# Performance work log

Measured on AMD Instinct MI355X. Metric: run time of the kernel, lower is better.

The kernel has to match this reference:

```python
import jax, jax.numpy as jnp
import numpy as np

B, L_SRC, L_TGT, H = 8, 256, 256, 768
N_SRC_WORDS, N_TGT_WORDS = 128, 128


def setup_inputs() -> dict:
    key = jax.random.key(0)
    k1, k2 = jax.random.split(key, 2)
    L = L_SRC + L_TGT
    tok_h = jax.random.normal(k1, (B, L, H), dtype=jnp.float32)
    attention_mask = jnp.ones((B, L), dtype=jnp.int32)
    # monotone word ids covering exactly N words (ragged spans of ~2 tokens/word)
    src_ids = (jnp.arange(L_SRC) * N_SRC_WORDS // L_SRC).astype(jnp.int64)
    tgt_ids = (jnp.arange(L_TGT) * N_TGT_WORDS // L_TGT).astype(jnp.int64)
    source_word_ids = jnp.broadcast_to(src_ids, (B, L_SRC))
    target_word_ids = jnp.broadcast_to(tgt_ids, (B, L_TGT))
    W = jax.random.normal(k2, (2 * H, 1), dtype=jnp.float32) * 0.02
    b = jnp.zeros((1,), dtype=jnp.float32)
    return dict(tok_h=tok_h, attention_mask=attention_mask,
                source_word_ids=source_word_ids, target_word_ids=target_word_ids,
                W=W, b=b, S=N_SRC_WORDS, T=N_TGT_WORDS)


def _pool_words(tok_h, combined_wid, attention_mask, n_words):
    """Vectorized equivalent of _pool_word_embeddings: mean over each
    contiguous run of equal word ids (masked / -1 tokens break runs)."""
    Bv, Lv, Hv = tok_h.shape
    valid = (attention_mask > 0) & (combined_wid >= 0)          # [B, L]
    prev_wid = jnp.pad(combined_wid[:, :-1], ((0, 0), (1, 0)), constant_values=-2)
    prev_valid = jnp.pad(valid[:, :-1], ((0, 0), (1, 0)), constant_values=False)
    new_run = valid & ((combined_wid != prev_wid) | (~prev_valid))
    run_id = jnp.cumsum(new_run.astype(jnp.int32), axis=1) - 1  # [B, L]
    n_seg = n_words + 1                                         # +1 dummy slot for invalid tokens
    seg = jnp.where(valid, run_id, n_words)
    gseg = (seg + jnp.arange(Bv, dtype=seg.dtype)[:, None] * n_seg).reshape(-1)
    sums = jax.ops.segment_sum(tok_h.reshape(Bv * Lv, Hv), gseg,
                               num_segments=Bv * n_seg).reshape(Bv, n_seg, Hv)
    counts = jax.ops.segment_sum(valid.astype(tok_h.dtype).reshape(-1), gseg,
                                 num_segments=Bv * n_seg).reshape(Bv, n_seg, 1)
    pooled = sums[:, :n_words] / jnp.maximum(counts[:, :n_words], 1.0)
    return pooled                                               # [B, n_words, H]


def reference(tok_h, attention_mask, source_word_ids, target_word_ids, W, b, S, T):
    combined_wid = jnp.concatenate([source_word_ids, target_word_ids], axis=1)  # [B, L]
    pooled = _pool_words(tok_h, combined_wid, attention_mask, S + T)            # [B, S+T, H]
    src = pooled[:, :S]            # [B, S, H]
    tgt = pooled[:, S:S + T]       # [B, T, H]
    # classifier(concat([src_exp, tgt_exp])) == src@W[:H] + tgt@W[H:] + b
    Hd = tok_h.shape[-1]
    w_src, w_tgt = W[:Hd, 0], W[Hd:, 0]
    logits = (src @ w_src)[:, :, None] + (tgt @ w_tgt)[:, None, :] + b[0]       # [B, S, T]
    return logits
```

## Files before the change

### kernel.cpp

```cpp
#include <hip/hip_runtime.h>
#include <hip/hip_bf16.h>

constexpr int B    = 8;
constexpr int LS   = 256;
constexpr int L    = 512;
constexpr int H    = 768;
constexpr int S    = 128;
constexpr int T    = 128;
constexpr int NW   = 256;

__global__ __launch_bounds__(256) void dot2_kernel(
    const float* __restrict__ tok, const float* __restrict__ Wp,
    float2* __restrict__ dvals)
{
    const int lane  = threadIdx.x & 63;
    const int wv    = threadIdx.x >> 6;
    const int token = blockIdx.x * 4 + wv;

    const float4* t4 = reinterpret_cast<const float4*>(tok + (size_t)token * H);
    const float4* s4 = reinterpret_cast<const float4*>(Wp);
    const float4* g4 = reinterpret_cast<const float4*>(Wp + H);

    float as = 0.f, at = 0.f;
    #pragma unroll
    for (int k = 0; k < 3; ++k) {
        const float4 a = t4[lane + 64 * k];
        const float4 s = s4[lane + 64 * k];
        const float4 g = g4[lane + 64 * k];
        as += a.x * s.x + a.y * s.y + a.z * s.z + a.w * s.w;
        at += a.x * g.x + a.y * g.y + a.z * g.z + a.w * g.w;
    }
    #pragma unroll
    for (int off = 32; off; off >>= 1) {
        as += __shfl_xor(as, off);
        at += __shfl_xor(at, off);
    }
    if (lane == 0) dvals[token] = make_float2(as, at);
}

__global__ __launch_bounds__(1024) void finalize_kernel(
    const int* __restrict__ mask, const int* __restrict__ sw,
    const int* __restrict__ tw, const float2* __restrict__ dvals,
    const float* __restrict__ bias, float* __restrict__ out)
{
    const int b   = blockIdx.x;
    const int tid = threadIdx.x;

    __shared__ int   sseg[L];
    __shared__ float lsum[NW + 1];
    __shared__ float lcnt[NW + 1];
    __shared__ float pooled[NW];

    if (tid < NW + 1) { lsum[tid] = 0.f; lcnt[tid] = 0.f; }
    __syncthreads();

    if (tid < 64) {
        const int lane = tid;
        const int base = lane * 8;

        int  wid[8]; bool val[8];
        #pragma unroll
        for (int j = 0; j < 8; ++j) {
            const int l = base + j;
            const int w = (l < LS) ? sw[b * LS + l] : tw[b * LS + (l - LS)];
            wid[j] = w;
            val[j] = (mask[b * L + l] > 0) && (w >= 0);
        }

        int pw = -2; bool pv = false;
        if (base > 0) {
            const int l = base - 1;
            pw = (l < LS) ? sw[b * LS + l] : tw[b * LS + (l - LS)];
            pv = (mask[b * L + l] > 0) && (pw >= 0);
        }

        int loc[8]; int c = 0;
        #pragma unroll
        for (int j = 0; j < 8; ++j) {
            const int nr = (val[j] && (wid[j] != pw || !pv)) ? 1 : 0;
            c += nr;
            loc[j] = c;
            pw = wid[j]; pv = val[j];
        }

        int inc = c;
        #pragma unroll
        for (int off = 1; off < 64; off <<= 1) {
            const int v = __shfl_up(inc, off);
            if (lane >= off) inc += v;
        }
        const int excl = inc - c;

        #pragma unroll
        for (int j = 0; j < 8; ++j) {
            const int rid = excl + loc[j] - 1;
            const int sg  = (val[j] && rid < NW) ? rid : NW;
            sseg[base + j] = sg;
            atomicAdd(&lcnt[sg], 1.0f);
        }
    }
    __syncthreads();

    if (tid < L) {
        const int sg = sseg[tid];
        if (sg < NW) {
            const float2 d = dvals[b * L + tid];
            atomicAdd(&lsum[sg], (sg < S) ? d.x : d.y);
        }
    }
    __syncthreads();

    if (tid < NW) pooled[tid] = lsum[tid] / fmaxf(lcnt[tid], 1.f);
    __syncthreads();

    const float b0 = bias[0];
    const int i  = tid >> 3;
    const int jb = (tid & 7) * 16;
    const float si = pooled[i] + b0;

    float4* o = reinterpret_cast<float4*>(out + (size_t)b * S * T + i * T + jb);
    #pragma unroll
    for (int j = 0; j < 16; j += 4) {
        float4 v;
        v.x = si + pooled[S + jb + j + 0];
        v.y = si + pooled[S + jb + j + 1];
        v.z = si + pooled[S + jb + j + 2];
        v.w = si + pooled[S + jb + j + 3];
        o[j >> 2] = v;
    }
}

extern "C" void kernel_launch(void* const* d_in, const int* in_sizes, int n_in,
                              void* d_out, int out_size, void* d_ws, size_t ws_size,
                              hipStream_t stream) {
    const float* tok  = (const float*)d_in[0];
    const int*   mask = (const int*)  d_in[1];
    const int*   sw   = (const int*)  d_in[2];
    const int*   tw   = (const int*)  d_in[3];
    const float* W    = (const float*)d_in[4];
    const float* bias = (const float*)d_in[5];
    float*       out  = (float*)d_out;

    float2* dvals = (float2*)d_ws;

    dot2_kernel<<<(B * L) / 4, 256, 0, stream>>>(tok, W, dvals);
    finalize_kernel<<<B, 1024, 0, stream>>>(mask, sw, tw, dvals, bias, out);
}
```

Before: 15.56 us.

## Fuse dot-product and pooling kernels into one cooperative kernel with grid sync

Merges the per-token dot-product kernel and the per-batch finalize kernel into one cooperative launch of 64 blocks of 1024 threads. Each block handles 64 tokens of one batch, computes segment ids and partial pooled sums in shared memory, writes the partials to workspace, then a grid-wide sync lets every block reduce the 8 partials and write its slice of the output. This removes one kernel launch and the global round trip of per-token dot values. In exchange only 64 blocks stream the 12 MB of token data, and the grid barrier and cooperative launch add their own cost.

```diff
diff --git a/kernel.cpp b/kernel.cpp
--- a/kernel.cpp
+++ b/kernel.cpp
@@ -1,64 +1,41 @@
 #include <hip/hip_runtime.h>
 #include <hip/hip_bf16.h>
+#include <hip/hip_cooperative_groups.h>
 
-constexpr int B    = 8;
-constexpr int LS   = 256;
-constexpr int L    = 512;
-constexpr int H    = 768;
-constexpr int S    = 128;
-constexpr int T    = 128;
-constexpr int NW   = 256;
+namespace cg = cooperative_groups;
 
-__global__ __launch_bounds__(256) void dot2_kernel(
-    const float* __restrict__ tok, const float* __restrict__ Wp,
-    float2* __restrict__ dvals)
+constexpr int B  = 8;
+constexpr int LS = 256;
+constexpr int L  = 512;
+constexpr int H  = 768;
+constexpr int S  = 128;
+constexpr int NW = 256;
+
+__global__ __launch_bounds__(1024) void fused_kernel(
+    const float* __restrict__ tok, const int* __restrict__ mask,
+    const int* __restrict__ sw, const int* __restrict__ tw,
+    const float* __restrict__ Wp, const float* __restrict__ bias,
+    float* __restrict__ out, float* __restrict__ psum)
 {
-    const int lane  = threadIdx.x & 63;
-    const int wv    = threadIdx.x >> 6;
-    const int token = blockIdx.x * 4 + wv;
+    const int g    = blockIdx.x;
+    const int b    = g >> 3;
+    const int s    = g & 7;
+    const int tid  = threadIdx.x;
+    const int lane = tid & 63;
+    const int wv   = tid >> 6;
 
-    const float4* t4 = reinterpret_cast<const float4*>(tok + (size_t)token * H);
-    const float4* s4 = reinterpret_cast<const float4*>(Wp);
-    const float4* g4 = reinterpret_cast<const float4*>(Wp + H);
+    __shared__ int    sseg[L];
+    __shared__ float2 dv[64];
+    __shared__ float  part[NW + 1];
+    __shared__ float  cnt[NW + 1];
+    __shared__ float  pooled[NW];
 
-    float as = 0.f, at = 0.f;
-    #pragma unroll
-    for (int k = 0; k < 3; ++k) {
-        const float4 a = t4[lane + 64 * k];
-        const float4 s = s4[lane + 64 * k];
-        const float4 g = g4[lane + 64 * k];
-        as += a.x * s.x + a.y * s.y + a.z * s.z + a.w * s.w;
-        at += a.x * g.x + a.y * g.y + a.z * g.z + a.w * g.w;
-    }
-    #pragma unroll
-    for (int off = 32; off; off >>= 1) {
-        as += __shfl_xor(as, off);
-        at += __shfl_xor(at, off);
-    }
-    if (lane == 0) dvals[token] = make_float2(as, at);
-}
-
-__global__ __launch_bounds__(1024) void finalize_kernel(
-    const int* __restrict__ mask, const int* __restrict__ sw,
-    const int* __restrict__ tw, const float2* __restrict__ dvals,
-    const float* __restrict__ bias, float* __restrict__ out)
-{
-    const int b   = blockIdx.x;
-    const int tid = threadIdx.x;
-
-    __shared__ int   sseg[L];
-    __shared__ float lsum[NW + 1];
-    __shared__ float lcnt[NW + 1];
-    __shared__ float pooled[NW];
-
-    if (tid < NW + 1) { lsum[tid] = 0.f; lcnt[tid] = 0.f; }
+    if (tid < NW + 1) { part[tid] = 0.f; cnt[tid] = 0.f; }
     __syncthreads();
 
-    if (tid < 64) {
-        const int lane = tid;
+    if (wv == 0) {
         const int base = lane * 8;
-
-        int  wid[8]; bool val[8];
+        int wid[8]; bool val[8];
         #pragma unroll
         for (int j = 0; j < 8; ++j) {
             const int l = base + j;
@@ -66,23 +43,18 @@
             wid[j] = w;
             val[j] = (mask[b * L + l] > 0) && (w >= 0);
         }
-
         int pw = -2; bool pv = false;
         if (base > 0) {
             const int l = base - 1;
             pw = (l < LS) ? sw[b * LS + l] : tw[b * LS + (l - LS)];
             pv = (mask[b * L + l] > 0) && (pw >= 0);
         }
-
         int loc[8]; int c = 0;
         #pragma unroll
         for (int j = 0; j < 8; ++j) {
             const int nr = (val[j] && (wid[j] != pw || !pv)) ? 1 : 0;
-            c += nr;
-            loc[j] = c;
-            pw = wid[j]; pv = val[j];
+            c += nr; loc[j] = c; pw = wid[j]; pv = val[j];
         }
-
         int inc = c;
         #pragma unroll
         for (int off = 1; off < 64; off <<= 1) {
@@ -90,43 +62,79 @@
             if (lane >= off) inc += v;
         }
         const int excl = inc - c;
-
         #pragma unroll
         for (int j = 0; j < 8; ++j) {
             const int rid = excl + loc[j] - 1;
             const int sg  = (val[j] && rid < NW) ? rid : NW;
             sseg[base + j] = sg;
-            atomicAdd(&lcnt[sg], 1.0f);
+            atomicAdd(&cnt[sg], 1.0f);
+        }
+    }
+
+    {
+        const float4* s4 = reinterpret_cast<const float4*>(Wp);
+        const float4* g4 = reinterpret_cast<const float4*>(Wp + H);
+        float4 wsv[3], wtv[3];
+        #pragma unroll
+        for (int k = 0; k < 3; ++k) {
+            wsv[k] = s4[lane + 64 * k];
+            wtv[k] = g4[lane + 64 * k];
+        }
+        #pragma unroll
+        for (int t = 0; t < 4; ++t) {
+            const int tl = wv * 4 + t;
+            const size_t tg = (size_t)b * L + s * 64 + tl;
+            const float4* t4 = reinterpret_cast<const float4*>(tok + tg * H);
+            float as = 0.f, at = 0.f;
+            #pragma unroll
+            for (int k = 0; k < 3; ++k) {
+                const float4 a = t4[lane + 64 * k];
+                as += a.x * wsv[k].x + a.y * wsv[k].y + a.z * wsv[k].z + a.w * wsv[k].w;
+                at += a.x * wtv[k].x + a.y * wtv[k].y + a.z * wtv[k].z + a.w * wtv[k].w;
+            }
+            #pragma unroll
+            for (int off = 32; off; off >>= 1) {
+                as += __shfl_xor(as, off);
+                at += __shfl_xor(at, off);
+            }
+            if (lane == 0) dv[tl] = make_float2(as, at);
         }
     }
     __syncthreads();
 
-    if (tid < L) {
-        const int sg = sseg[tid];
+    if (tid < 64) {
+        const int sg = sseg[s * 64 + tid];
         if (sg < NW) {
-            const float2 d = dvals[b * L + tid];
-            atomicAdd(&lsum[sg], (sg < S) ? d.x : d.y);
+            const float2 d = dv[tid];
+            atomicAdd(&part[sg], (sg < S) ? d.x : d.y);
         }
     }
     __syncthreads();
 
-    if (tid < NW) pooled[tid] = lsum[tid] / fmaxf(lcnt[tid], 1.f);
+    if (tid < NW) psum[g * NW + tid] = part[tid];
+    __threadfence();
+
+    cg::this_grid().sync();
+
+    if (tid < NW) {
+        float acc = 0.f;
+        #pragma unroll
+        for (int k = 0; k < 8; ++k) acc += psum[(b * 8 + k) * NW + tid];
+        pooled[tid] = acc / fmaxf(cnt[tid], 1.f);
+    }
     __syncthreads();
 
-    const float b0 = bias[0];
-    const int i  = tid >> 3;
-    const int jb = (tid & 7) * 16;
-    const float si = pooled[i] + b0;
-
-    float4* o = reinterpret_cast<float4*>(out + (size_t)b * S * T + i * T + jb);
-    #pragma unroll
-    for (int j = 0; j < 16; j += 4) {
+    if (tid < 512) {
+        const float b0 = bias[0];
+        const int r = s * 16 + (tid >> 5);
+        const int c = (tid & 31) * 4;
+        const float si = pooled[r] + b0;
         float4 v;
-        v.x = si + pooled[S + jb + j + 0];
-        v.y = si + pooled[S + jb + j + 1];
-        v.z = si + pooled[S + jb + j + 2];
-        v.w = si + pooled[S + jb + j + 3];
-        o[j >> 2] = v;
+        v.x = si + pooled[S + c + 0];
+        v.y = si + pooled[S + c + 1];
+        v.z = si + pooled[S + c + 2];
+        v.w = si + pooled[S + c + 3];
+        *reinterpret_cast<float4*>(out + (size_t)b * S * 128 + r * 128 + c) = v;
     }
 }
 
@@ -140,9 +148,10 @@
     const float* W    = (const float*)d_in[4];
     const float* bias = (const float*)d_in[5];
     float*       out  = (float*)d_out;
+    float*       psum = (float*)d_ws;
 
-    float2* dvals = (float2*)d_ws;
-
-    dot2_kernel<<<(B * L) / 4, 256, 0, stream>>>(tok, W, dvals);
-    finalize_kernel<<<B, 1024, 0, stream>>>(mask, sw, tw, dvals, bias, out);
+    void* args[] = { (void*)&tok, (void*)&mask, (void*)&sw, (void*)&tw,
+                     (void*)&W, (void*)&bias, (void*)&out, (void*)&psum };
+    hipLaunchCooperativeKernel(reinterpret_cast<void*>(fused_kernel),
+                               dim3(64), dim3(1024), args, 0, stream);
 }
```

Measured after the change: 52.61 us. 3.38x slower.

## Process four tokens per wave in dot kernel and split finalize across 64 blocks

Applied to the files above, without the earlier changes.

The dot kernel now has each wavefront handle four tokens, loading the classifier weights into registers once and reusing them, which cuts the grid from 1024 to 256 blocks. The finalize kernel moves from 8 blocks of 1024 threads to 64 blocks of 256 threads. Each block redoes the segment scan and pooling for its batch and then writes a 16-row slice of the output. This spreads the output writes over more CUs at the cost of repeating the pooling work eight times per batch. Fewer dot blocks also means less parallelism for streaming the 12 MB activation tensor.

```diff
diff --git a/kernel.cpp b/kernel.cpp
--- a/kernel.cpp
+++ b/kernel.cpp
@@ -1,49 +1,57 @@
 #include <hip/hip_runtime.h>
 #include <hip/hip_bf16.h>
 
-constexpr int B    = 8;
-constexpr int LS   = 256;
-constexpr int L    = 512;
-constexpr int H    = 768;
-constexpr int S    = 128;
-constexpr int T    = 128;
-constexpr int NW   = 256;
+constexpr int B  = 8;
+constexpr int LS = 256;
+constexpr int L  = 512;
+constexpr int H  = 768;
+constexpr int S  = 128;
+constexpr int NW = 256;
 
 __global__ __launch_bounds__(256) void dot2_kernel(
     const float* __restrict__ tok, const float* __restrict__ Wp,
     float2* __restrict__ dvals)
 {
-    const int lane  = threadIdx.x & 63;
-    const int wv    = threadIdx.x >> 6;
-    const int token = blockIdx.x * 4 + wv;
+    const int lane = threadIdx.x & 63;
+    const int wv   = threadIdx.x >> 6;
+    const int t0   = (blockIdx.x * 4 + wv) * 4;
 
-    const float4* t4 = reinterpret_cast<const float4*>(tok + (size_t)token * H);
     const float4* s4 = reinterpret_cast<const float4*>(Wp);
     const float4* g4 = reinterpret_cast<const float4*>(Wp + H);
-
-    float as = 0.f, at = 0.f;
+    float4 wsv[3], wtv[3];
     #pragma unroll
     for (int k = 0; k < 3; ++k) {
-        const float4 a = t4[lane + 64 * k];
-        const float4 s = s4[lane + 64 * k];
-        const float4 g = g4[lane + 64 * k];
-        as += a.x * s.x + a.y * s.y + a.z * s.z + a.w * s.w;
-        at += a.x * g.x + a.y * g.y + a.z * g.z + a.w * g.w;
+        wsv[k] = s4[lane + 64 * k];
+        wtv[k] = g4[lane + 64 * k];
     }
+
     #pragma unroll
-    for (int off = 32; off; off >>= 1) {
-        as += __shfl_xor(as, off);
-        at += __shfl_xor(at, off);
+    for (int t = 0; t < 4; ++t) {
+        const float4* t4 = reinterpret_cast<const float4*>(tok + (size_t)(t0 + t) * H);
+        float as = 0.f, at = 0.f;
+        #pragma unroll
+        for (int k = 0; k < 3; ++k) {
+            const float4 a = t4[lane + 64 * k];
+            as += a.x * wsv[k].x + a.y * wsv[k].y + a.z * wsv[k].z + a.w * wsv[k].w;
+            at += a.x * wtv[k].x + a.y * wtv[k].y + a.z * wtv[k].z + a.w * wtv[k].w;
+        }
+        #pragma unroll
+        for (int off = 32; off; off >>= 1) {
+            as += __shfl_xor(as, off);
+            at += __shfl_xor(at, off);
+        }
+        if (lane == 0) dvals[t0 + t] = make_float2(as, at);
     }
-    if (lane == 0) dvals[token] = make_float2(as, at);
 }
 
-__global__ __launch_bounds__(1024) void finalize_kernel(
+__global__ __launch_bounds__(256) void finalize_kernel(
     const int* __restrict__ mask, const int* __restrict__ sw,
     const int* __restrict__ tw, const float2* __restrict__ dvals,
     const float* __restrict__ bias, float* __restrict__ out)
 {
-    const int b   = blockIdx.x;
+    const int g   = blockIdx.x;
+    const int b   = g >> 3;
+    const int s   = g & 7;
     const int tid = threadIdx.x;
 
     __shared__ int   sseg[L];
@@ -57,8 +65,7 @@
     if (tid < 64) {
         const int lane = tid;
         const int base = lane * 8;
-
-        int  wid[8]; bool val[8];
+        int wid[8]; bool val[8];
         #pragma unroll
         for (int j = 0; j < 8; ++j) {
             const int l = base + j;
@@ -66,23 +73,18 @@
             wid[j] = w;
             val[j] = (mask[b * L + l] > 0) && (w >= 0);
         }
-
         int pw = -2; bool pv = false;
         if (base > 0) {
             const int l = base - 1;
             pw = (l < LS) ? sw[b * LS + l] : tw[b * LS + (l - LS)];
             pv = (mask[b * L + l] > 0) && (pw >= 0);
         }
-
         int loc[8]; int c = 0;
         #pragma unroll
         for (int j = 0; j < 8; ++j) {
             const int nr = (val[j] && (wid[j] != pw || !pv)) ? 1 : 0;
-            c += nr;
-            loc[j] = c;
-            pw = wid[j]; pv = val[j];
+            c += nr; loc[j] = c; pw = wid[j]; pv = val[j];
         }
-
         int inc = c;
         #pragma unroll
         for (int off = 1; off < 64; off <<= 1) {
@@ -90,7 +92,6 @@
             if (lane >= off) inc += v;
         }
         const int excl = inc - c;
-
         #pragma unroll
         for (int j = 0; j < 8; ++j) {
             const int rid = excl + loc[j] - 1;
@@ -101,10 +102,12 @@
     }
     __syncthreads();
 
-    if (tid < L) {
-        const int sg = sseg[tid];
+    #pragma unroll
+    for (int r = 0; r < 2; ++r) {
+        const int tl = tid + r * 256;
+        const int sg = sseg[tl];
         if (sg < NW) {
-            const float2 d = dvals[b * L + tid];
+            const float2 d = dvals[b * L + tl];
             atomicAdd(&lsum[sg], (sg < S) ? d.x : d.y);
         }
     }
@@ -114,18 +117,18 @@
     __syncthreads();
 
     const float b0 = bias[0];
-    const int i  = tid >> 3;
-    const int jb = (tid & 7) * 16;
-    const float si = pooled[i] + b0;
+    const int r = s * 16 + (tid >> 4);
+    const int c = (tid & 15) * 8;
+    const float si = pooled[r] + b0;
 
-    float4* o = reinterpret_cast<float4*>(out + (size_t)b * S * T + i * T + jb);
+    float4* o = reinterpret_cast<float4*>(out + (size_t)b * S * 128 + r * 128 + c);
     #pragma unroll
-    for (int j = 0; j < 16; j += 4) {
+    for (int j = 0; j < 8; j += 4) {
         float4 v;
-        v.x = si + pooled[S + jb + j + 0];
-        v.y = si + pooled[S + jb + j + 1];
-        v.z = si + pooled[S + jb + j + 2];
-        v.w = si + pooled[S + jb + j + 3];
+        v.x = si + pooled[S + c + j + 0];
+        v.y = si + pooled[S + c + j + 1];
+        v.z = si + pooled[S + c + j + 2];
+        v.w = si + pooled[S + c + j + 3];
         o[j >> 2] = v;
     }
 }
@@ -143,6 +146,6 @@
 
     float2* dvals = (float2*)d_ws;
 
-    dot2_kernel<<<(B * L) / 4, 256, 0, stream>>>(tok, W, dvals);
-    finalize_kernel<<<B, 1024, 0, stream>>>(mask, sw, tw, dvals, bias, out);
+    dot2_kernel<<<256, 256, 0, stream>>>(tok, W, dvals);
+    finalize_kernel<<<64, 256, 0, stream>>>(mask, sw, tw, dvals, bias, out);
 }
```

Measured after the change: 14.31 us. 8.1% less time.
